# Performance work log

Hardware: AMD Instinct MI355X
Metric: run time of the kernel (lower is better)

Reference implementation:

```python
import jax, jax.numpy as jnp
import numpy as np

B, T, H = 4096, 512, 256


def setup_inputs() -> dict:
    key = jax.random.key(0)
    ks = jax.random.split(key, 10)
    s = 0.05
    return {
        "x": jax.random.normal(ks[0], (B, T, 1), dtype=jnp.float32),
        "eps": jax.random.normal(ks[1], (B, T, 1), dtype=jnp.float32),  # randn_like noise, pregenerated
        "w_ih": jax.random.normal(ks[2], (4 * H, 1), dtype=jnp.float32) * s,
        "w_hh": jax.random.normal(ks[3], (4 * H, H), dtype=jnp.float32) * s,
        "b_ih": jax.random.normal(ks[4], (4 * H,), dtype=jnp.float32) * s,
        "b_hh": jax.random.normal(ks[5], (4 * H,), dtype=jnp.float32) * s,
        "w_mean": jax.random.normal(ks[6], (1, H), dtype=jnp.float32) * s,
        "b_mean": jax.random.normal(ks[7], (1,), dtype=jnp.float32) * s,
        "w_logvar": jax.random.normal(ks[8], (1, H), dtype=jnp.float32) * s,
        "b_logvar": jax.random.normal(ks[9], (1,), dtype=jnp.float32) * s,
    }


def reference(x, eps, w_ih, w_hh, b_ih, b_hh, w_mean, b_mean, w_logvar, b_logvar):
    """Teacher-forcing forward: per-step LSTMCell + mean/logvar heads + reparam sample.
    Returns (outputs, means, logvars), each [B, T, 1]."""
    b = x.shape[0]
    h0 = jnp.zeros((b, H), dtype=x.dtype)
    c0 = jnp.zeros((b, H), dtype=x.dtype)

    def step(carry, inp):
        h, c = carry
        xt, et = inp  # [B,1] each
        # PyTorch LSTMCell: gates ordered (i, f, g, o)
        gates = xt @ w_ih.T + b_ih + h @ w_hh.T + b_hh  # [B, 4H]
        i, f, g, o = jnp.split(gates, 4, axis=-1)
        i = jax.nn.sigmoid(i)
        f = jax.nn.sigmoid(f)
        g = jnp.tanh(g)
        o = jax.nn.sigmoid(o)
        c = f * c + i * g
        h = o * jnp.tanh(c)
        mean = h @ w_mean.T + b_mean            # [B, 1]
        logvar = jnp.clip(h @ w_logvar.T + b_logvar, -10.0, 2.0)
        sample = mean + jnp.exp(0.5 * logvar) * et
        return (h, c), (sample, mean, logvar)

    xs = (jnp.swapaxes(x, 0, 1), jnp.swapaxes(eps, 0, 1))  # time-major [T,B,1]
    _, (s, m, lv) = jax.lax.scan(step, (h0, c0), xs)
    to_bt = lambda a: jnp.swapaxes(a, 0, 1)  # back to [B,T,1]
    return to_bt(s), to_bt(m), to_bt(lv)
```

## Files before the change

### kernel.cpp

```cpp
#include <hip/hip_runtime.h>
#include <hip/hip_bf16.h>

#define BB 4096
#define TT 512
#define HH 256

typedef __bf16 bf16x8 __attribute__((ext_vector_type(8)));
typedef __bf16 bf16x4 __attribute__((ext_vector_type(4)));
typedef float f32x4 __attribute__((ext_vector_type(4)));
typedef long fp8frag;

#define MFMA_BF16 __builtin_amdgcn_mfma_f32_16x16x32_bf16
#define MFMA_FP8  __builtin_amdgcn_mfma_f32_16x16x32_fp8_fp8

#if defined(__has_builtin)
#if __has_builtin(__builtin_amdgcn_exp2f)
#define EXP2F(x) __builtin_amdgcn_exp2f(x)
#endif
#endif
#ifndef EXP2F
#define EXP2F(x) __expf((x) * 0.6931471805599453f)
#endif
#define RCPF(x) __builtin_amdgcn_rcpf(x)

#define L2E  1.4426950408889634f
#define TL2E 2.8853900817779268f
#define HL2E 0.7213475204444817f

__global__ void prep_weights8(const float* __restrict__ w_hh, const float* __restrict__ w_ih,
                              const float* __restrict__ b_ih, const float* __restrict__ b_hh,
                              char* __restrict__ wB8) {
    int idx = blockIdx.x * blockDim.x + threadIdx.x;
    if (idx >= 64 * 9 * 64) return;
    int l = idx & 63;
    int kt = (idx >> 6) % 9;
    int ctg = idx / (9 * 64);
    int n = ctg * 16 + (l & 15);
    int k0 = kt * 32 + 8 * (l >> 4);
    float f[8];
#pragma unroll
    for (int e = 0; e < 8; ++e) {
        int k = k0 + e;
        float v = 0.f;
        if (k < 256) v = w_hh[n * HH + k];
        else if (k == 256) v = w_ih[n];
        else if (k == 257) v = b_ih[n] + b_hh[n];
        f[e] = v * 64.f;
    }
    int lo = __builtin_amdgcn_cvt_pk_fp8_f32(f[0], f[1], 0, false);
    lo = __builtin_amdgcn_cvt_pk_fp8_f32(f[2], f[3], lo, true);
    int hi = __builtin_amdgcn_cvt_pk_fp8_f32(f[4], f[5], 0, false);
    hi = __builtin_amdgcn_cvt_pk_fp8_f32(f[6], f[7], hi, true);
    int2 v; v.x = lo; v.y = hi;
    *(int2*)(wB8 + (size_t)idx * 8) = v;
}

#define SGg(v) RCPF(1.f + EXP2F(-(v)))
#define THg(v) (1.f - 2.f * RCPF(EXP2F(v) + 1.f))

__global__ __launch_bounds__(512, 1) void lstm_fused(
    const float* __restrict__ x, const float* __restrict__ eps,
    const float* __restrict__ w_mean, const float* __restrict__ b_mean,
    const float* __restrict__ w_logvar, const float* __restrict__ b_logvar,
    const char* __restrict__ wB8, float* __restrict__ out)
{
    __shared__ __align__(16) char wlds8[8][27][512];
    __shared__ __align__(16) __bf16 hbuf[2][16][296];
    __shared__ __align__(16) char hbuf8[2][16][296];
    __shared__ __align__(16) __bf16 headw[9][512];
    __shared__ float obuf[2][16][16];

    const int tid = threadIdx.x;
    const int w = tid >> 6;
    const int l = tid & 63;
    const int m0 = blockIdx.x * 16;

    for (int i = tid; i < 2 * 16 * 296; i += 512) (&hbuf[0][0][0])[i] = (__bf16)0.f;
    for (int i = tid; i < 2 * 16 * 296; i += 512) (&hbuf8[0][0][0])[i] = 0;
    for (int i = tid; i < 9 * 64; i += 512) {
        int kt = i >> 6, hl = i & 63;
        int col = hl & 15;
        int k0 = kt * 32 + 8 * (hl >> 4);
        bf16x8 hw;
#pragma unroll
        for (int e = 0; e < 8; ++e) {
            int k = k0 + e;
            float v = 0.f;
            if (k < 256) {
                if (col == 0) v = w_mean[k];
                else if (col == 1) v = w_logvar[k];
            } else if (k == 257) {
                if (col == 0) v = b_mean[0];
                else if (col == 1) v = b_logvar[0];
            }
            hw[e] = (__bf16)v;
        }
        *(bf16x8*)&headw[kt][hl * 8] = hw;
    }

    fp8frag wreg8[36];
#pragma unroll
    for (int kt = 0; kt < 9; ++kt) {
        wreg8[kt]      = *(const fp8frag*)(wB8 + ((size_t)((w)      * 9 + kt) * 64 + l) * 8);
        wreg8[9 + kt]  = *(const fp8frag*)(wB8 + ((size_t)((w + 16) * 9 + kt) * 64 + l) * 8);
        wreg8[18 + kt] = *(const fp8frag*)(wB8 + ((size_t)((w + 8)  * 9 + kt) * 64 + l) * 8);
        wreg8[27 + kt] = *(const fp8frag*)(wB8 + ((size_t)((w + 24) * 9 + kt) * 64 + l) * 8);
        *(fp8frag*)&wlds8[w][kt][l * 8] =
            *(const fp8frag*)(wB8 + ((size_t)((w + 32) * 9 + kt) * 64 + l) * 8);
        *(fp8frag*)&wlds8[w][9 + kt][l * 8] =
            *(const fp8frag*)(wB8 + ((size_t)((w + 48) * 9 + kt) * 64 + l) * 8);
        *(fp8frag*)&wlds8[w][18 + kt][l * 8] =
            *(const fp8frag*)(wB8 + ((size_t)((w + 40) * 9 + kt) * 64 + l) * 8);
    }
    const char* pc7 = wB8 + ((size_t)((w + 56) * 9 + 4) * 64 + l) * 8;

    const int arow = l & 15;
    const int ako = 8 * (l >> 4);
    const int u0 = 16 * w + ((l >> 4) << 2);
    const int u1 = u0 + 128;

    const float DS1c = L2E / 1024.f;
    const float DS2c = TL2E / 1024.f;

    float c[8];
#pragma unroll
    for (int i = 0; i < 8; ++i) c[i] = 0.f;
    const f32x4 Z = {0.f, 0.f, 0.f, 0.f};

    __syncthreads();
    if (tid < 16) {
        hbuf[0][tid][257] = (__bf16)1.0f;
        hbuf[1][tid][257] = (__bf16)1.0f;
        hbuf8[0][tid][257] = (char)__builtin_amdgcn_cvt_pk_fp8_f32(16.f, 0.f, 0, false);
        hbuf8[1][tid][257] = (char)__builtin_amdgcn_cvt_pk_fp8_f32(16.f, 0.f, 0, false);
        float x0 = x[(size_t)(m0 + tid) * TT];
        hbuf[1][tid][256] = (__bf16)x0;
        hbuf8[1][tid][256] = (char)__builtin_amdgcn_cvt_pk_fp8_f32(x0 * 16.f, 0.f, 0, false);
    }
    fp8frag sbf = *(const fp8frag*)(pc7 - 2048);
    fp8frag tbf;
    __syncthreads();

#define P0KT(KT, RB)                                                            \
    do {                                                                        \
        fp8frag hf_ = *(const fp8frag*)&hbuf8[RB][arow][(KT) * 32 + ako];       \
        a0 = MFMA_FP8(wreg8[KT], hf_, (KT) ? a0 : Z, 0, 0, 0);                  \
        a1 = MFMA_FP8(wreg8[9 + (KT)], hf_, (KT) ? a1 : Z, 0, 0, 0);            \
        a2 = MFMA_FP8(*(const fp8frag*)&wlds8[w][KT][l * 8], hf_, (KT) ? a2 : Z, 0, 0, 0);       \
        a3 = MFMA_FP8(*(const fp8frag*)&wlds8[w][9 + (KT)][l * 8], hf_, (KT) ? a3 : Z, 0, 0, 0); \
    } while (0)

#define P1KT(KT, NXT, RB, USE, PF)                                              \
    do {                                                                        \
        fp8frag hf_ = *(const fp8frag*)&hbuf8[RB][arow][(KT) * 32 + ako];       \
        PF = *(const fp8frag*)(pc7 + ((NXT) - 4) * 512);                        \
        a4 = MFMA_FP8(wreg8[18 + (KT)], hf_, (KT) ? a4 : Z, 0, 0, 0);           \
        a5 = MFMA_FP8(wreg8[27 + (KT)], hf_, (KT) ? a5 : Z, 0, 0, 0);           \
        a6 = MFMA_FP8(*(const fp8frag*)&wlds8[w][18 + (KT)][l * 8], hf_, (KT) ? a6 : Z, 0, 0, 0);\
        a7 = MFMA_FP8(USE, hf_, (KT) ? a7 : Z, 0, 0, 0);                        \
    } while (0)

#define EWP0C(J)                                                                \
    do {                                                                        \
        float gi_ = a0[J] * DS1c, gf_ = a1[J] * DS1c;                           \
        float gg_ = a2[J] * DS2c, go_ = a3[J] * DS1c;                           \
        float cn_ = fmaf(SGg(gf_), c[J], SGg(gi_) * THg(gg_));                  \
        c[J] = cn_;                                                             \
        hA[J] = SGg(go_) * THg(cn_ * TL2E);                                     \
    } while (0)

#define EWP1C(J)                                                                \
    do {                                                                        \
        float gi_ = a4[J] * DS1c, gf_ = a5[J] * DS1c;                           \
        float gg_ = a6[J] * DS2c, go_ = a7[J] * DS1c;                           \
        float cn_ = fmaf(SGg(gf_), c[4 + (J)], SGg(gi_) * THg(gg_));            \
        c[4 + (J)] = cn_;                                                       \
        hB[J] = SGg(go_) * THg(cn_ * TL2E);                                     \
    } while (0)

#define WRH(PB, HV, U)                                                          \
    do {                                                                        \
        bf16x4 hb_ = {(__bf16)HV[0], (__bf16)HV[1], (__bf16)HV[2], (__bf16)HV[3]};\
        *(bf16x4*)&hbuf[PB][arow][U] = hb_;                                     \
        int pk_ = __builtin_amdgcn_cvt_pk_fp8_f32(HV[0] * 16.f, HV[1] * 16.f, 0, false);\
        pk_ = __builtin_amdgcn_cvt_pk_fp8_f32(HV[2] * 16.f, HV[3] * 16.f, pk_, true);  \
        *(int*)&hbuf8[PB][arow][U] = pk_;                                       \
    } while (0)

#define HEADS(RB, SLOT)                                                         \
    do {                                                                        \
        f32x4 ah_;                                                              \
        {                                                                       \
            bf16x8 hb_ = *(const bf16x8*)&hbuf[RB][arow][0 * 32 + ako];         \
            ah_ = MFMA_BF16(*(const bf16x8*)&headw[0][l * 8], hb_, Z, 0, 0, 0); \
        }                                                                       \
        _Pragma("unroll")                                                       \
        for (int kt_ = 1; kt_ < 9; ++kt_) {                                     \
            bf16x8 hb_ = *(const bf16x8*)&hbuf[RB][arow][kt_ * 32 + ako];       \
            ah_ = MFMA_BF16(*(const bf16x8*)&headw[kt_][l * 8], hb_, ah_, 0, 0, 0);\
        }                                                                       \
        if (l < 16) {                                                           \
            obuf[0][l][SLOT] = ah_[0];                                          \
            obuf[1][l][SLOT] = fminf(fmaxf(ah_[1], -10.f), 2.f);                \
        }                                                                       \
    } while (0)

#define FLUSH(T0)                                                               \
    do {                                                                        \
        if (tid < 192) {                                                        \
            const int o_ = tid >> 6, rr_ = (tid >> 2) & 15, q_ = tid & 3;       \
            f32x4 mv_ = *(const f32x4*)&obuf[0][rr_][q_ * 4];                   \
            f32x4 lv_ = *(const f32x4*)&obuf[1][rr_][q_ * 4];                   \
            const size_t base_ = (size_t)(m0 + rr_) * TT + (T0) + q_ * 4;       \
            if (o_ == 0) {                                                      \
                f32x4 e_ = *(const f32x4*)&eps[base_];                          \
                f32x4 s_;                                                       \
                _Pragma("unroll")                                               \
                for (int k_ = 0; k_ < 4; ++k_)                                  \
                    s_[k_] = fmaf(EXP2F(lv_[k_] * HL2E), e_[k_], mv_[k_]);      \
                *(f32x4*)&out[base_] = s_;                                      \
            } else if (o_ == 1) {                                               \
                *(f32x4*)&out[(size_t)BB * TT + base_] = mv_;                   \
            } else {                                                            \
                *(f32x4*)&out[2 * (size_t)BB * TT + base_] = lv_;               \
            }                                                                   \
        }                                                                       \
    } while (0)

#define STEP(PB, RB, BA, BX)                                                    \
    do {                                                                        \
        const int tt = t0 + (PB);                                               \
        float xn = 0.f;                                                         \
        if (tid < 16 && tt + 1 < TT) xn = x[(size_t)(m0 + tid) * TT + (tt + 1)];\
        f32x4 a0, a1, a2, a3, a4, a5, a6, a7;                                   \
        float hA[4], hB[4];                                                     \
        P0KT(0, RB); P0KT(1, RB); P0KT(2, RB); P0KT(3, RB); P0KT(4, RB);        \
        P0KT(5, RB); P0KT(6, RB); P0KT(7, RB); P0KT(8, RB);                     \
        P1KT(0, 1, RB, BA, BX); P1KT(1, 2, RB, BX, BA); EWP0C(0);               \
        P1KT(2, 3, RB, BA, BX); P1KT(3, 4, RB, BX, BA); EWP0C(1);               \
        P1KT(4, 5, RB, BA, BX); P1KT(5, 6, RB, BX, BA); EWP0C(2);               \
        P1KT(6, 7, RB, BA, BX); P1KT(7, 8, RB, BX, BA); EWP0C(3);               \
        P1KT(8, 0, RB, BA, BX);                                                 \
        WRH(PB, hA, u0);                                                        \
        if (w == 7 && tt >= 1) { HEADS(RB, (tt - 1) & 15); }                    \
        EWP1C(0); EWP1C(1); EWP1C(2); EWP1C(3);                                 \
        WRH(PB, hB, u1);                                                        \
        if (tid < 16 && tt + 1 < TT) {                                          \
            hbuf[PB][tid][256] = (__bf16)xn;                                    \
            hbuf8[PB][tid][256] =                                               \
                (char)__builtin_amdgcn_cvt_pk_fp8_f32(xn * 16.f, 0.f, 0, false);\
        }                                                                       \
        if ((PB) == 0 && tt > 0 && (tt & 15) == 0) {                            \
            __syncthreads();                                                    \
            FLUSH(tt - 16);                                                     \
        }                                                                       \
        __syncthreads();                                                        \
    } while (0)

    for (int t0 = 0; t0 < TT; t0 += 2) {
        STEP(0, 1, sbf, tbf);
        STEP(1, 0, tbf, sbf);
    }

    if (w == 7) { HEADS(1, 15); }
    __syncthreads();
    FLUSH(TT - 16);

#undef P0KT
#undef P1KT
#undef EWP0C
#undef EWP1C
#undef WRH
#undef HEADS
#undef FLUSH
#undef STEP
}

extern "C" void kernel_launch(void* const* d_in, const int* in_sizes, int n_in,
                              void* d_out, int out_size, void* d_ws, size_t ws_size,
                              hipStream_t stream) {
    const float* x = (const float*)d_in[0];
    const float* eps = (const float*)d_in[1];
    const float* w_ih = (const float*)d_in[2];
    const float* w_hh = (const float*)d_in[3];
    const float* b_ih = (const float*)d_in[4];
    const float* b_hh = (const float*)d_in[5];
    const float* w_mean = (const float*)d_in[6];
    const float* b_mean = (const float*)d_in[7];
    const float* w_logvar = (const float*)d_in[8];
    const float* b_logvar = (const float*)d_in[9];

    char* wB8 = (char*)d_ws;

    prep_weights8<<<144, 256, 0, stream>>>(w_hh, w_ih, b_ih, b_hh, wB8);
    lstm_fused<<<256, 512, 0, stream>>>(x, eps, w_mean, b_mean, w_logvar, b_logvar,
                                        wB8, (float*)d_out);
}
```

Before: 1.068 ms.

## Use 16x16x128 scaled FP8 MFMA with all recurrent weights held in registers

Result: faster. 880.8 us (-17.5%).

```diff
diff --git a/kernel.cpp b/kernel.cpp
--- a/kernel.cpp
+++ b/kernel.cpp
@@ -8,10 +8,14 @@
 typedef __bf16 bf16x8 __attribute__((ext_vector_type(8)));
 typedef __bf16 bf16x4 __attribute__((ext_vector_type(4)));
 typedef float f32x4 __attribute__((ext_vector_type(4)));
+typedef int i32x8 __attribute__((ext_vector_type(8)));
 typedef long fp8frag;
 
 #define MFMA_BF16 __builtin_amdgcn_mfma_f32_16x16x32_bf16
 #define MFMA_FP8  __builtin_amdgcn_mfma_f32_16x16x32_fp8_fp8
+#define MFMA_SC(A, B, C) \
+    __builtin_amdgcn_mfma_scale_f32_16x16x128_f8f6f4( \
+        A, B, C, 0, 0, 0, 0x7F7F7F7F, 0, 0x7F7F7F7F)
 
 #if defined(__has_builtin)
 #if __has_builtin(__builtin_amdgcn_exp2f)
@@ -31,28 +35,45 @@
                               const float* __restrict__ b_ih, const float* __restrict__ b_hh,
                               char* __restrict__ wB8) {
     int idx = blockIdx.x * blockDim.x + threadIdx.x;
-    if (idx >= 64 * 9 * 64) return;
-    int l = idx & 63;
-    int kt = (idx >> 6) % 9;
-    int ctg = idx / (9 * 64);
-    int n = ctg * 16 + (l & 15);
-    int k0 = kt * 32 + 8 * (l >> 4);
-    float f[8];
-#pragma unroll
-    for (int e = 0; e < 8; ++e) {
-        int k = k0 + e;
-        float v = 0.f;
-        if (k < 256) v = w_hh[n * HH + k];
-        else if (k == 256) v = w_ih[n];
-        else if (k == 257) v = b_ih[n] + b_hh[n];
-        f[e] = v * 64.f;
-    }
-    int lo = __builtin_amdgcn_cvt_pk_fp8_f32(f[0], f[1], 0, false);
-    lo = __builtin_amdgcn_cvt_pk_fp8_f32(f[2], f[3], lo, true);
-    int hi = __builtin_amdgcn_cvt_pk_fp8_f32(f[4], f[5], 0, false);
-    hi = __builtin_amdgcn_cvt_pk_fp8_f32(f[6], f[7], hi, true);
-    int2 v; v.x = lo; v.y = hi;
-    *(int2*)(wB8 + (size_t)idx * 8) = v;
+    if (idx < 64 * 2 * 64) {
+        int l = idx & 63;
+        int kb = (idx >> 6) & 1;
+        int ctg = idx >> 7;
+        int n = ctg * 16 + (l & 15);
+        int k0 = kb * 128 + (l >> 4) * 32;
+        const float* src = w_hh + n * HH + k0;
+        i32x8 v;
+#pragma unroll
+        for (int d = 0; d < 8; ++d) {
+            int pk = __builtin_amdgcn_cvt_pk_fp8_f32(src[4 * d] * 64.f,
+                                                     src[4 * d + 1] * 64.f, 0, false);
+            pk = __builtin_amdgcn_cvt_pk_fp8_f32(src[4 * d + 2] * 64.f,
+                                                 src[4 * d + 3] * 64.f, pk, true);
+            v[d] = pk;
+        }
+        *(i32x8*)(wB8 + (size_t)idx * 32) = v;
+    } else if (idx < 64 * 2 * 64 + 64 * 64) {
+        int j = idx - 64 * 2 * 64;
+        int l = j & 63;
+        int ctg = j >> 6;
+        int n = ctg * 16 + (l & 15);
+        int k0 = 256 + 8 * (l >> 4);
+        float f[8];
+#pragma unroll
+        for (int e = 0; e < 8; ++e) {
+            int k = k0 + e;
+            float v = 0.f;
+            if (k == 256) v = w_ih[n];
+            else if (k == 257) v = b_ih[n] + b_hh[n];
+            f[e] = v * 64.f;
+        }
+        int lo = __builtin_amdgcn_cvt_pk_fp8_f32(f[0], f[1], 0, false);
+        lo = __builtin_amdgcn_cvt_pk_fp8_f32(f[2], f[3], lo, true);
+        int hi = __builtin_amdgcn_cvt_pk_fp8_f32(f[4], f[5], 0, false);
+        hi = __builtin_amdgcn_cvt_pk_fp8_f32(f[6], f[7], hi, true);
+        int2 v2; v2.x = lo; v2.y = hi;
+        *(int2*)(wB8 + 262144 + (size_t)j * 8) = v2;
+    }
 }
 
 #define SGg(v) RCPF(1.f + EXP2F(-(v)))
@@ -64,9 +85,8 @@
     const float* __restrict__ w_logvar, const float* __restrict__ b_logvar,
     const char* __restrict__ wB8, float* __restrict__ out)
 {
-    __shared__ __align__(16) char wlds8[8][27][512];
     __shared__ __align__(16) __bf16 hbuf[2][16][296];
-    __shared__ __align__(16) char hbuf8[2][16][296];
+    __shared__ __align__(16) char hbuf8[2][16][304];
     __shared__ __align__(16) __bf16 headw[9][512];
     __shared__ float obuf[2][16][16];
 
@@ -76,7 +96,7 @@
     const int m0 = blockIdx.x * 16;
 
     for (int i = tid; i < 2 * 16 * 296; i += 512) (&hbuf[0][0][0])[i] = (__bf16)0.f;
-    for (int i = tid; i < 2 * 16 * 296; i += 512) (&hbuf8[0][0][0])[i] = 0;
+    for (int i = tid; i < 2 * 16 * 304; i += 512) (&hbuf8[0][0][0])[i] = 0;
     for (int i = tid; i < 9 * 64; i += 512) {
         int kt = i >> 6, hl = i & 63;
         int col = hl & 15;
@@ -98,24 +118,20 @@
         *(bf16x8*)&headw[kt][hl * 8] = hw;
     }
 
-    fp8frag wreg8[36];
-#pragma unroll
-    for (int kt = 0; kt < 9; ++kt) {
-        wreg8[kt]      = *(const fp8frag*)(wB8 + ((size_t)((w)      * 9 + kt) * 64 + l) * 8);
-        wreg8[9 + kt]  = *(const fp8frag*)(wB8 + ((size_t)((w + 16) * 9 + kt) * 64 + l) * 8);
-        wreg8[18 + kt] = *(const fp8frag*)(wB8 + ((size_t)((w + 8)  * 9 + kt) * 64 + l) * 8);
-        wreg8[27 + kt] = *(const fp8frag*)(wB8 + ((size_t)((w + 24) * 9 + kt) * 64 + l) * 8);
-        *(fp8frag*)&wlds8[w][kt][l * 8] =
-            *(const fp8frag*)(wB8 + ((size_t)((w + 32) * 9 + kt) * 64 + l) * 8);
-        *(fp8frag*)&wlds8[w][9 + kt][l * 8] =
-            *(const fp8frag*)(wB8 + ((size_t)((w + 48) * 9 + kt) * 64 + l) * 8);
-        *(fp8frag*)&wlds8[w][18 + kt][l * 8] =
-            *(const fp8frag*)(wB8 + ((size_t)((w + 40) * 9 + kt) * 64 + l) * 8);
-    }
-    const char* pc7 = wB8 + ((size_t)((w + 56) * 9 + 4) * 64 + l) * 8;
+    i32x8 wbig[16];
+    fp8frag wsm[8];
+#pragma unroll
+    for (int cc = 0; cc < 8; ++cc) {
+        const int ctg = w + 8 * (cc >> 2) + 16 * (cc & 3);
+        wbig[2 * cc]     = *(const i32x8*)(wB8 + ((size_t)(ctg * 2 + 0) * 64 + l) * 32);
+        wbig[2 * cc + 1] = *(const i32x8*)(wB8 + ((size_t)(ctg * 2 + 1) * 64 + l) * 32);
+        wsm[cc] = *(const fp8frag*)(wB8 + 262144 + ((size_t)ctg * 64 + l) * 8);
+    }
 
     const int arow = l & 15;
-    const int ako = 8 * (l >> 4);
+    const int a32 = 32 * (l >> 4);
+    const int ak8 = 8 * (l >> 4);
+    const int ako = 16 * (l >> 4);
     const int u0 = 16 * w + ((l >> 4) << 2);
     const int u1 = u0 + 128;
 
@@ -137,30 +153,9 @@
         hbuf[1][tid][256] = (__bf16)x0;
         hbuf8[1][tid][256] = (char)__builtin_amdgcn_cvt_pk_fp8_f32(x0 * 16.f, 0.f, 0, false);
     }
-    fp8frag sbf = *(const fp8frag*)(pc7 - 2048);
-    fp8frag tbf;
     __syncthreads();
 
-#define P0KT(KT, RB)                                                            \
-    do {                                                                        \
-        fp8frag hf_ = *(const fp8frag*)&hbuf8[RB][arow][(KT) * 32 + ako];       \
-        a0 = MFMA_FP8(wreg8[KT], hf_, (KT) ? a0 : Z, 0, 0, 0);                  \
-        a1 = MFMA_FP8(wreg8[9 + (KT)], hf_, (KT) ? a1 : Z, 0, 0, 0);            \
-        a2 = MFMA_FP8(*(const fp8frag*)&wlds8[w][KT][l * 8], hf_, (KT) ? a2 : Z, 0, 0, 0);       \
-        a3 = MFMA_FP8(*(const fp8frag*)&wlds8[w][9 + (KT)][l * 8], hf_, (KT) ? a3 : Z, 0, 0, 0); \
-    } while (0)
-
-#define P1KT(KT, NXT, RB, USE, PF)                                              \
-    do {                                                                        \
-        fp8frag hf_ = *(const fp8frag*)&hbuf8[RB][arow][(KT) * 32 + ako];       \
-        PF = *(const fp8frag*)(pc7 + ((NXT) - 4) * 512);                        \
-        a4 = MFMA_FP8(wreg8[18 + (KT)], hf_, (KT) ? a4 : Z, 0, 0, 0);           \
-        a5 = MFMA_FP8(wreg8[27 + (KT)], hf_, (KT) ? a5 : Z, 0, 0, 0);           \
-        a6 = MFMA_FP8(*(const fp8frag*)&wlds8[w][18 + (KT)][l * 8], hf_, (KT) ? a6 : Z, 0, 0, 0);\
-        a7 = MFMA_FP8(USE, hf_, (KT) ? a7 : Z, 0, 0, 0);                        \
-    } while (0)
-
-#define EWP0C(J)                                                                \
+#define EWAC(J)                                                                 \
     do {                                                                        \
         float gi_ = a0[J] * DS1c, gf_ = a1[J] * DS1c;                           \
         float gg_ = a2[J] * DS2c, go_ = a3[J] * DS1c;                           \
@@ -169,7 +164,7 @@
         hA[J] = SGg(go_) * THg(cn_ * TL2E);                                     \
     } while (0)
 
-#define EWP1C(J)                                                                \
+#define EWBC(J)                                                                 \
     do {                                                                        \
         float gi_ = a4[J] * DS1c, gf_ = a5[J] * DS1c;                           \
         float gg_ = a6[J] * DS2c, go_ = a7[J] * DS1c;                           \
@@ -191,12 +186,12 @@
     do {                                                                        \
         f32x4 ah_;                                                              \
         {                                                                       \
-            bf16x8 hb_ = *(const bf16x8*)&hbuf[RB][arow][0 * 32 + ako];         \
+            bf16x8 hb_ = *(const bf16x8*)&hbuf[RB][arow][0 * 32 + ako / 2];     \
             ah_ = MFMA_BF16(*(const bf16x8*)&headw[0][l * 8], hb_, Z, 0, 0, 0); \
         }                                                                       \
         _Pragma("unroll")                                                       \
         for (int kt_ = 1; kt_ < 9; ++kt_) {                                     \
-            bf16x8 hb_ = *(const bf16x8*)&hbuf[RB][arow][kt_ * 32 + ako];       \
+            bf16x8 hb_ = *(const bf16x8*)&hbuf[RB][arow][kt_ * 32 + ako / 2];   \
             ah_ = MFMA_BF16(*(const bf16x8*)&headw[kt_][l * 8], hb_, ah_, 0, 0, 0);\
         }                                                                       \
         if (l < 16) {                                                           \
@@ -227,23 +222,41 @@
         }                                                                       \
     } while (0)
 
-#define STEP(PB, RB, BA, BX)                                                    \
+#define STEP(PB, RB)                                                            \
     do {                                                                        \
         const int tt = t0 + (PB);                                               \
         float xn = 0.f;                                                         \
         if (tid < 16 && tt + 1 < TT) xn = x[(size_t)(m0 + tid) * TT + (tt + 1)];\
+        i32x8 hf0 = *(const i32x8*)&hbuf8[RB][arow][a32];                       \
+        i32x8 hf1 = *(const i32x8*)&hbuf8[RB][arow][128 + a32];                 \
+        fp8frag hf8 = *(const fp8frag*)&hbuf8[RB][arow][256 + ak8];             \
         f32x4 a0, a1, a2, a3, a4, a5, a6, a7;                                   \
         float hA[4], hB[4];                                                     \
-        P0KT(0, RB); P0KT(1, RB); P0KT(2, RB); P0KT(3, RB); P0KT(4, RB);        \
-        P0KT(5, RB); P0KT(6, RB); P0KT(7, RB); P0KT(8, RB);                     \
-        P1KT(0, 1, RB, BA, BX); P1KT(1, 2, RB, BX, BA); EWP0C(0);               \
-        P1KT(2, 3, RB, BA, BX); P1KT(3, 4, RB, BX, BA); EWP0C(1);               \
-        P1KT(4, 5, RB, BA, BX); P1KT(5, 6, RB, BX, BA); EWP0C(2);               \
-        P1KT(6, 7, RB, BA, BX); P1KT(7, 8, RB, BX, BA); EWP0C(3);               \
-        P1KT(8, 0, RB, BA, BX);                                                 \
+                  \
+        a0 = MFMA_SC(wbig[0], hf0, Z);  a1 = MFMA_SC(wbig[2], hf0, Z);          \
+        a2 = MFMA_SC(wbig[4], hf0, Z);  a3 = MFMA_SC(wbig[6], hf0, Z);          \
+        a0 = MFMA_SC(wbig[1], hf1, a0); a1 = MFMA_SC(wbig[3], hf1, a1);         \
+        a2 = MFMA_SC(wbig[5], hf1, a2); a3 = MFMA_SC(wbig[7], hf1, a3);         \
+        a0 = MFMA_FP8(wsm[0], hf8, a0, 0, 0, 0);                                \
+        a1 = MFMA_FP8(wsm[1], hf8, a1, 0, 0, 0);                                \
+        a2 = MFMA_FP8(wsm[2], hf8, a2, 0, 0, 0);                                \
+        a3 = MFMA_FP8(wsm[3], hf8, a3, 0, 0, 0);                                \
+                         \
+        a4 = MFMA_SC(wbig[8], hf0, Z);  a5 = MFMA_SC(wbig[10], hf0, Z);         \
+        a6 = MFMA_SC(wbig[12], hf0, Z); a7 = MFMA_SC(wbig[14], hf0, Z);         \
+        EWAC(0);                                                                \
+        a4 = MFMA_SC(wbig[9], hf1, a4); a5 = MFMA_SC(wbig[11], hf1, a5);        \
+        EWAC(1);                                                                \
+        a6 = MFMA_SC(wbig[13], hf1, a6); a7 = MFMA_SC(wbig[15], hf1, a7);       \
+        EWAC(2);                                                                \
+        a4 = MFMA_FP8(wsm[4], hf8, a4, 0, 0, 0);                                \
+        a5 = MFMA_FP8(wsm[5], hf8, a5, 0, 0, 0);                                \
+        a6 = MFMA_FP8(wsm[6], hf8, a6, 0, 0, 0);                                \
+        a7 = MFMA_FP8(wsm[7], hf8, a7, 0, 0, 0);                                \
+        EWAC(3);                                                                \
         WRH(PB, hA, u0);                                                        \
         if (w == 7 && tt >= 1) { HEADS(RB, (tt - 1) & 15); }                    \
-        EWP1C(0); EWP1C(1); EWP1C(2); EWP1C(3);                                 \
+        EWBC(0); EWBC(1); EWBC(2); EWBC(3);                                     \
         WRH(PB, hB, u1);                                                        \
         if (tid < 16 && tt + 1 < TT) {                                          \
             hbuf[PB][tid][256] = (__bf16)xn;                                    \
@@ -258,18 +271,16 @@
     } while (0)
 
     for (int t0 = 0; t0 < TT; t0 += 2) {
-        STEP(0, 1, sbf, tbf);
-        STEP(1, 0, tbf, sbf);
+        STEP(0, 1);
+        STEP(1, 0);
     }
 
     if (w == 7) { HEADS(1, 15); }
     __syncthreads();
     FLUSH(TT - 16);
 
-#undef P0KT
-#undef P1KT
-#undef EWP0C
-#undef EWP1C
+#undef EWAC
+#undef EWBC
 #undef WRH
 #undef HEADS
 #undef FLUSH
@@ -292,7 +303,7 @@
 
     char* wB8 = (char*)d_ws;
 
-    prep_weights8<<<144, 256, 0, stream>>>(w_hh, w_ih, b_ih, b_hh, wB8);
+    prep_weights8<<<48, 256, 0, stream>>>(w_hh, w_ih, b_ih, b_hh, wB8);
     lstm_fused<<<256, 512, 0, stream>>>(x, eps, w_mean, b_mean, w_logvar, b_logvar,
                                         wB8, (float*)d_out);
 }
```
